# Optimization experiments

Hardware: AMD Instinct MI355X
Metric: run time of the kernel (lower is better)

The kernel has to match this reference:

```python
import jax, jax.numpy as jnp
import numpy as np

HID = 3584; NH = 16; NKV = 8; HD = 256; S = 3072; WIN = 2048
SOFTCAP = 50.0; QSCALE = 256.0 ** -0.5  # query_pre_attn_scalar = 256
NEG = -2.3819763e38


def _rope(x, cos, sin):
    # x: (B, S, heads, HD); cos/sin: (S, HD//2). Gemma half-split complex RoPE.
    x1, x2 = jnp.split(x, 2, axis=-1)
    c = cos[None, :, None, :]
    s = sin[None, :, None, :]
    return jnp.concatenate([x1 * c - x2 * s, x1 * s + x2 * c], axis=-1)


def setup_inputs() -> dict:
    key = jax.random.key(0)
    k1, k2, k3 = jax.random.split(key, 3)
    hidden_states = jax.random.normal(k1, (1, S, HID), jnp.float32)
    qkv_w = jax.random.normal(k2, (NH * HD + 2 * NKV * HD, HID), jnp.float32) * 0.02
    o_w = jax.random.normal(k3, (HID, NH * HD), jnp.float32) * 0.02
    inv = 1.0 / (10000.0 ** (jnp.arange(0, HD, 2, dtype=jnp.float32) / HD))
    ang = jnp.arange(S, dtype=jnp.float32)[:, None] * inv[None, :]
    freqs_cis = jnp.stack([jnp.cos(ang), jnp.sin(ang)], axis=-1)  # (S, HD//2, 2)
    kv_write_indices = jnp.arange(S, dtype=jnp.int32)
    k_cache = jnp.zeros((1, S, NKV, HD), jnp.float32)
    v_cache = jnp.zeros((1, S, NKV, HD), jnp.float32)
    i = jnp.arange(S)[:, None]
    j = jnp.arange(S)[None, :]
    mask = jnp.where(j <= i, 0.0, NEG).astype(jnp.float32)[None, None]  # causal (1,1,S,S)
    return dict(hidden_states=hidden_states, freqs_cis=freqs_cis,
                kv_write_indices=kv_write_indices, k_cache=k_cache, v_cache=v_cache,
                mask=mask, qkv_w=qkv_w, o_w=o_w)


def reference(hidden_states, freqs_cis, kv_write_indices, k_cache, v_cache, mask, qkv_w, o_w):
    B, L, _ = hidden_states.shape
    qkv = hidden_states @ qkv_w.T  # (B, L, 8192)
    xq, xk, xv = jnp.split(qkv, [NH * HD, NH * HD + NKV * HD], axis=-1)
    xq = xq.reshape(B, L, NH, HD)
    xk = xk.reshape(B, L, NKV, HD)
    xv = xv.reshape(B, L, NKV, HD)
    cos, sin = freqs_cis[..., 0], freqs_cis[..., 1]
    xq = _rope(xq, cos, sin)
    xk = _rope(xk, cos, sin)
    # KV cache index_copy_ on dim 1
    k_all = k_cache.at[:, kv_write_indices].set(xk)  # (B, T, NKV, HD)
    v_all = v_cache.at[:, kv_write_indices].set(xv)
    T = k_all.shape[1]
    G = NH // NKV  # queries per kv head; grouped einsum avoids repeat_interleave
    q = (xq * QSCALE).transpose(0, 2, 1, 3).reshape(B, NKV, G, L, HD)
    k = k_all.transpose(0, 2, 1, 3)  # (B, NKV, T, HD)
    v = v_all.transpose(0, 2, 1, 3)
    scores = jnp.einsum('bkgsd,bktd->bkgst', q, k)
    # logit softcapping
    scores = jnp.tanh(scores / SOFTCAP) * SOFTCAP
    # sliding-window band applied on top of the provided (causal) mask
    i = jnp.arange(L)[:, None]
    j = jnp.arange(T)[None, :]
    band = (j >= i - WIN + 1) & (j <= i + WIN - 1)
    m = jnp.where(band, mask, NEG)  # (1,1,L,T)
    scores = scores + m[:, :, None]  # broadcast over group dim
    probs = jax.nn.softmax(scores.astype(jnp.float32), axis=-1).astype(q.dtype)
    out = jnp.einsum('bkgst,bktd->bkgsd', probs, v)
    out = out.reshape(B, NH, L, HD).transpose(0, 2, 1, 3).reshape(B, L, NH * HD)
    return out @ o_w.T
```

## Files before the change

kernel.cpp:

```cpp
#include <hip/hip_runtime.h>

#define S_LEN 3072
#define NHQ 16
#define NKVH 8
#define HDIM 256
#define WIN 2048
#define QKV_COLS 8192

typedef __bf16 bf16x8 __attribute__((ext_vector_type(8)));
typedef float f32x4 __attribute__((ext_vector_type(4)));

__device__ __forceinline__ unsigned short f2bf(float f) {
    union { float f; unsigned u; } v; v.f = f;
    unsigned r = v.u + 0x7FFFu + ((v.u >> 16) & 1u);
    return (unsigned short)(r >> 16);
}
__device__ __forceinline__ float bf2f(unsigned short u) {
    union { unsigned u; float f; } v; v.u = ((unsigned)u) << 16; return v.f;
}

typedef __attribute__((address_space(3))) void lds_void_t;
typedef const __attribute__((address_space(1))) void glb_void_t;
__device__ __forceinline__ void async16(const void* g, void* l) {
    __builtin_amdgcn_global_load_lds((glb_void_t*)g, (lds_void_t*)l, 16, 0, 0);
}

__global__ __launch_bounds__(256) void cast_bf16_kernel(const float* __restrict__ src,
                                                        unsigned short* __restrict__ dst,
                                                        int n) {
    int i = (blockIdx.x * 256 + threadIdx.x) * 4;
    if (i >= n) return;
    float4 v = *(const float4*)(src + i);
    ushort4 o;
    o.x = f2bf(v.x); o.y = f2bf(v.y); o.z = f2bf(v.z); o.w = f2bf(v.w);
    *(ushort4*)(dst + i) = o;
}

template <int OUT_BF16>
__global__ __launch_bounds__(256) void gemm_bt(const unsigned short* __restrict__ A,
                                               const unsigned short* __restrict__ B,
                                               void* __restrict__ Cv,
                                               int N, int K) {
    __shared__ __align__(16) unsigned short At[128 * 32];
    __shared__ __align__(16) unsigned short Bt[128 * 32];
    const int tid = threadIdx.x;
    const int wid = tid >> 6, lane = tid & 63;
    const int ln = lane & 15, quad = lane >> 4;
    const int bm = blockIdx.y, bn = blockIdx.x;
    const int wm = wid >> 1, wn = wid & 1;

    const f32x4 fzero = {0.f, 0.f, 0.f, 0.f};
    f32x4 acc[4][4];
#pragma unroll
    for (int i = 0; i < 4; i++) {
#pragma unroll
        for (int j = 0; j < 4; j++) acc[i][j] = fzero;
    }

    const unsigned short* gA = A + (size_t)(bm * 128 + wid * 32 + (lane >> 2)) * K + (lane & 3) * 8;
    const unsigned short* gB = B + (size_t)(bn * 128 + wid * 32 + (lane >> 2)) * K + (lane & 3) * 8;
    unsigned short* lA = At + wid * 32 * 32;
    unsigned short* lB = Bt + wid * 32 * 32;

    for (int k0 = 0; k0 < K; k0 += 32) {
        async16(gA + k0, lA);
        async16(gA + k0 + 16 * K, lA + 16 * 32);
        async16(gB + k0, lB);
        async16(gB + k0 + 16 * K, lB + 16 * 32);
        __syncthreads();

        bf16x8 af[4], bfr[4];
#pragma unroll
        for (int mt = 0; mt < 4; mt++)
            af[mt] = *(const bf16x8*)(At + (wm * 64 + mt * 16 + ln) * 32 + quad * 8);
#pragma unroll
        for (int nt = 0; nt < 4; nt++)
            bfr[nt] = *(const bf16x8*)(Bt + (wn * 64 + nt * 16 + ln) * 32 + quad * 8);
#pragma unroll
        for (int mt = 0; mt < 4; mt++) {
#pragma unroll
            for (int nt = 0; nt < 4; nt++)
                acc[mt][nt] = __builtin_amdgcn_mfma_f32_16x16x32_bf16(af[mt], bfr[nt], acc[mt][nt], 0, 0, 0);
        }
        __syncthreads();
    }

    const int row0 = bm * 128 + wm * 64 + quad * 4;
    const int col0 = bn * 128 + wn * 64 + ln;
    if (OUT_BF16) {
        unsigned short* C = (unsigned short*)Cv;
#pragma unroll
        for (int mt = 0; mt < 4; mt++) {
#pragma unroll
            for (int nt = 0; nt < 4; nt++) {
#pragma unroll
                for (int rr = 0; rr < 4; rr++)
                    C[(size_t)(row0 + mt * 16 + rr) * N + col0 + nt * 16] = f2bf(acc[mt][nt][rr]);
            }
        }
    } else {
        float* C = (float*)Cv;
#pragma unroll
        for (int mt = 0; mt < 4; mt++) {
#pragma unroll
            for (int nt = 0; nt < 4; nt++) {
#pragma unroll
                for (int rr = 0; rr < 4; rr++)
                    C[(size_t)(row0 + mt * 16 + rr) * N + col0 + nt * 16] = acc[mt][nt][rr];
            }
        }
    }
}

__global__ __launch_bounds__(256) void rope_kernel(const unsigned short* __restrict__ qkv,
                                                   const float* __restrict__ freqs,
                                                   const int* __restrict__ kvidx,
                                                   unsigned short* __restrict__ Qb,
                                                   unsigned short* __restrict__ Kb) {
    int t = blockIdx.x * 256 + threadIdx.x;
    int d = t & 127;
    int t2 = t >> 7;
    int hh = t2 % 24;
    int pos = t2 / 24;
    if (pos >= S_LEN) return;
    float2 cs = *(const float2*)(freqs + ((size_t)pos * 128 + d) * 2);
    if (hh < NHQ) {
        const unsigned short* src = qkv + (size_t)pos * QKV_COLS + hh * HDIM + d;
        float x1 = bf2f(src[0]), x2 = bf2f(src[128]);
        float o1 = (x1 * cs.x - x2 * cs.y) * 0.0625f;
        float o2 = (x1 * cs.y + x2 * cs.x) * 0.0625f;
        unsigned short* dst = Qb + ((size_t)hh * S_LEN + pos) * HDIM + d;
        dst[0] = f2bf(o1);
        dst[128] = f2bf(o2);
    } else {
        int kvh = hh - NHQ;
        const unsigned short* src = qkv + (size_t)pos * QKV_COLS + NHQ * HDIM + kvh * HDIM + d;
        float x1 = bf2f(src[0]), x2 = bf2f(src[128]);
        float o1 = x1 * cs.x - x2 * cs.y;
        float o2 = x1 * cs.y + x2 * cs.x;
        int wpos = kvidx[pos];
        unsigned short* dst = Kb + ((size_t)kvh * S_LEN + wpos) * HDIM + d;
        dst[0] = f2bf(o1);
        dst[128] = f2bf(o2);
    }
}

__global__ __launch_bounds__(256) void vtrans_kernel(const unsigned short* __restrict__ qkv,
                                                     const int* __restrict__ kvidx,
                                                     unsigned short* __restrict__ Vbt) {
    __shared__ unsigned short T[64][72];
    int pos0 = blockIdx.x * 64;
    int c0 = blockIdx.y * 64;
    int a = threadIdx.x >> 6;
    int b = threadIdx.x & 63;
#pragma unroll
    for (int r = 0; r < 16; r++) {
        int pl = r * 4 + a;
        T[pl][b] = qkv[(size_t)(pos0 + pl) * QKV_COLS + 6144 + c0 + b];
    }
    __syncthreads();
    int wpos = kvidx[pos0 + b];
#pragma unroll
    for (int r = 0; r < 16; r++) {
        int cl = r * 4 + a;
        Vbt[(size_t)(c0 + cl) * S_LEN + wpos] = T[b][cl];
    }
}

__global__ __launch_bounds__(256) void attn_kernel(const unsigned short* __restrict__ Qb,
                                                   const unsigned short* __restrict__ Kb,
                                                   const unsigned short* __restrict__ Vbt,
                                                   float* __restrict__ Acc,
                                                   float* __restrict__ Ps,
                                                   unsigned short* __restrict__ attn_out) {
    __shared__ __align__(16) unsigned short Kl[32][264];
    __shared__ __align__(16) unsigned short Vt[256][40];
    __shared__ __align__(16) unsigned short Pl[4][16][40];

    const int h = blockIdx.x / 96;
    const int it = 95 - (blockIdx.x % 96);
    int qb, sub, nc;
    if (it < 16)      { qb = it; sub = 0; nc = 1; }
    else if (it < 48) { int e = it - 16; qb = 16 + (e >> 1); sub = e & 1; nc = 2; }
    else              { int e = it - 48; qb = 32 + e / 3; sub = e % 3; nc = 3; }

    const int kv = h >> 1;
    const int q0 = qb * 64;
    const int tid = threadIdx.x;
    const int wid = tid >> 6, lane = tid & 63;
    const int ln = lane & 15, quad = lane >> 4;

    bf16x8 qf[8];
    {
        const unsigned short* qrow = Qb + ((size_t)h * S_LEN + q0 + wid * 16 + ln) * HDIM;
#pragma unroll
        for (int k0 = 0; k0 < 8; k0++)
            qf[k0] = *(const bf16x8*)(qrow + k0 * 32 + quad * 8);
    }

    const f32x4 fzero = {0.f, 0.f, 0.f, 0.f};
    f32x4 acc[16];
#pragma unroll
    for (int t = 0; t < 16; t++) acc[t] = fzero;
    float ps[4] = {0.f, 0.f, 0.f, 0.f};

    const int imin = q0 + wid * 16;
    const int imax = imin + 15;
    const int irow = imin + quad * 4;

    const int t_lo = (q0 >= WIN) ? ((q0 - (WIN - 1)) >> 5) : 0;
    const int t_hi = (q0 + 63) >> 5;
    const int tn = t_hi - t_lo + 1;
    const int ts = t_lo + (tn * sub) / nc;
    const int te = t_lo + (tn * (sub + 1)) / nc;

    const int krow = tid >> 3, kcs = (tid & 7) * 32;
    const unsigned short* ksrc0 = Kb + ((size_t)kv * S_LEN + krow) * HDIM + kcs;
    const unsigned short* vsrc0 = Vbt + ((size_t)kv * HDIM + tid) * S_LEN;

    for (int tt = ts; tt < te; tt++) {
        const int p0 = tt * 32;
        {
            const unsigned short* ks = ksrc0 + (size_t)p0 * HDIM;
            unsigned short* kd = &Kl[krow][kcs];
#pragma unroll
            for (int j = 0; j < 4; j++)
                *(uint4*)(kd + j * 8) = *(const uint4*)(ks + j * 8);
            const unsigned short* vs = vsrc0 + p0;
            unsigned short* vd = &Vt[tid][0];
#pragma unroll
            for (int j = 0; j < 4; j++)
                *(uint4*)(vd + j * 8) = *(const uint4*)(vs + j * 8);
        }
        __syncthreads();

        const bool live = (p0 <= imax) && (p0 + 31 >= imin - WIN + 1);
        if (live) {
            f32x4 s0 = fzero, s1 = fzero;
#pragma unroll
            for (int k0 = 0; k0 < 8; k0++) {
                bf16x8 b0 = *(const bf16x8*)(&Kl[ln][k0 * 32 + quad * 8]);
                s0 = __builtin_amdgcn_mfma_f32_16x16x32_bf16(qf[k0], b0, s0, 0, 0, 0);
            }
#pragma unroll
            for (int k0 = 0; k0 < 8; k0++) {
                bf16x8 b1 = *(const bf16x8*)(&Kl[16 + ln][k0 * 32 + quad * 8]);
                s1 = __builtin_amdgcn_mfma_f32_16x16x32_bf16(qf[k0], b1, s1, 0, 0, 0);
            }

            const bool full = (p0 + 31 <= imin) && (p0 >= imax - WIN + 1);
#pragma unroll
            for (int r = 0; r < 4; r++) {
                float z0 = __expf(s0[r] * 0.04f);
                float z1 = __expf(s1[r] * 0.04f);
                float t0 = fmaf(-100.f, __builtin_amdgcn_rcpf(z0 + 1.f), 50.f);
                float t1 = fmaf(-100.f, __builtin_amdgcn_rcpf(z1 + 1.f), 50.f);
                float p0v = __expf(t0);
                float p1v = __expf(t1);
                if (!full) {
                    const int i = irow + r;
                    int j0 = p0 + ln, j1 = p0 + 16 + ln;
                    p0v = ((j0 <= i) && (j0 + WIN > i)) ? p0v : 0.f;
                    p1v = ((j1 <= i) && (j1 + WIN > i)) ? p1v : 0.f;
                }
                ps[r] += p0v + p1v;
                Pl[wid][quad * 4 + r][ln] = f2bf(p0v);
                Pl[wid][quad * 4 + r][16 + ln] = f2bf(p1v);
            }
            bf16x8 pa = *(const bf16x8*)(&Pl[wid][ln][quad * 8]);
#pragma unroll
            for (int t = 0; t < 16; t++) {
                bf16x8 vb = *(const bf16x8*)(&Vt[t * 16 + ln][quad * 8]);
                acc[t] = __builtin_amdgcn_mfma_f32_16x16x32_bf16(pa, vb, acc[t], 0, 0, 0);
            }
        }
        __syncthreads();
    }

    float psr[4];
#pragma unroll
    for (int r = 0; r < 4; r++) {
        float s = ps[r];
#pragma unroll
        for (int o = 1; o <= 8; o <<= 1)
            s += __shfl_xor(s, o);
        psr[r] = s;
    }

    if (nc == 1) {
#pragma unroll
        for (int t = 0; t < 16; t++) {
#pragma unroll
            for (int r = 0; r < 4; r++) {
                float o = acc[t][r] * __builtin_amdgcn_rcpf(psr[r]);
                attn_out[(size_t)(irow + r) * 4096 + h * HDIM + t * 16 + ln] = f2bf(o);
            }
        }
    } else {
        if (ln == 0) {
#pragma unroll
            for (int r = 0; r < 4; r++)
                atomicAdd(&Ps[h * S_LEN + irow + r], psr[r]);
        }
#pragma unroll
        for (int t = 0; t < 16; t++) {
#pragma unroll
            for (int r = 0; r < 4; r++)
                atomicAdd(&Acc[((size_t)h * S_LEN + irow + r) * HDIM + t * 16 + ln], acc[t][r]);
        }
    }
}

__global__ __launch_bounds__(256) void norm_kernel(const float* __restrict__ Acc,
                                                   const float* __restrict__ Ps,
                                                   unsigned short* __restrict__ attn_out) {
    int row = blockIdx.x * 4 + (threadIdx.x >> 6);
    int lane = threadIdx.x & 63;
    int h = row >> 11;
    int pos = 1024 + (row & 2047);
    float4 a = *(const float4*)(Acc + ((size_t)h * S_LEN + pos) * HDIM + lane * 4);
    float inv = __builtin_amdgcn_rcpf(Ps[h * S_LEN + pos]);
    ushort4 o;
    o.x = f2bf(a.x * inv); o.y = f2bf(a.y * inv);
    o.z = f2bf(a.z * inv); o.w = f2bf(a.w * inv);
    *(ushort4*)(attn_out + (size_t)pos * 4096 + h * HDIM + lane * 4) = o;
}

extern "C" void kernel_launch(void* const* d_in, const int* in_sizes, int n_in,
                              void* d_out, int out_size, void* d_ws, size_t ws_size,
                              hipStream_t stream) {
    (void)in_sizes; (void)n_in; (void)out_size; (void)ws_size;
    const float* hidden = (const float*)d_in[0];
    const float* freqs  = (const float*)d_in[1];
    const int* kvidx    = (const int*)d_in[2];
    const float* qkv_w  = (const float*)d_in[6];
    const float* o_w    = (const float*)d_in[7];
    float* out = (float*)d_out;

    char* ws = (char*)d_ws;
    unsigned short* hs_bf   = (unsigned short*)(ws);
    unsigned short* w1_bf   = (unsigned short*)(ws + 22020096);
    unsigned short* w2_bf   = (unsigned short*)(ws + 80740352);
    unsigned short* qkv_bf  = (unsigned short*)(ws + 110100480);
    unsigned short* Qb      = (unsigned short*)(ws + 160432128);
    unsigned short* Kb      = (unsigned short*)(ws + 185597952);
    unsigned short* Vbt     = (unsigned short*)(ws + 198180864);
    unsigned short* attn_bf = (unsigned short*)(ws + 210763776);

    float* Acc = (float*)(ws + 110100480);
    float* Ps  = (float*)(ws);

    cast_bf16_kernel<<<10752, 256, 0, stream>>>(hidden, hs_bf, 11010048);
    cast_bf16_kernel<<<28672, 256, 0, stream>>>(qkv_w, w1_bf, 29360128);
    cast_bf16_kernel<<<14336, 256, 0, stream>>>(o_w, w2_bf, 14680064);

    gemm_bt<1><<<dim3(64, 24), 256, 0, stream>>>(hs_bf, w1_bf, (void*)qkv_bf, 8192, 3584);

    rope_kernel<<<36864, 256, 0, stream>>>(qkv_bf, freqs, kvidx, Qb, Kb);
    vtrans_kernel<<<dim3(48, 32), 256, 0, stream>>>(qkv_bf, kvidx, Vbt);

    hipMemsetAsync(Acc, 0, (size_t)16 * 3072 * 256 * 4, stream);
    hipMemsetAsync(Ps, 0, (size_t)16 * 3072 * 4, stream);

    attn_kernel<<<1536, 256, 0, stream>>>(Qb, Kb, Vbt, Acc, Ps, attn_bf);
    norm_kernel<<<8192, 256, 0, stream>>>(Acc, Ps, attn_bf);

    gemm_bt<0><<<dim3(28, 24), 256, 0, stream>>>(attn_bf, w2_bf, (void*)out, 3584, 4096);
}
```

Baseline: 942.7 us.

## Make attention waves independent with 32-row tiles reading K/V directly from global

Restructures the attention kernel so each wave owns a 32-query-row tile and loads K and V fragments straight from global memory instead of staging them through shared memory. This removes the block-wide __syncthreads barriers. The work split now uses up to 5 KV chunks per tile, and the norm kernel covers the extra rows that need reduction. In exchange, each wave holds more registers (two Q fragment sets and two accumulator sets), relies on L2/cache for K/V reuse across waves, and does more atomic adds.

```diff
diff --git a/kernel.cpp b/kernel.cpp
--- a/kernel.cpp
+++ b/kernel.cpp
@@ -167,124 +167,121 @@
     }
 }
 
-__global__ __launch_bounds__(256) void attn_kernel(const unsigned short* __restrict__ Qb,
-                                                   const unsigned short* __restrict__ Kb,
-                                                   const unsigned short* __restrict__ Vbt,
-                                                   float* __restrict__ Acc,
-                                                   float* __restrict__ Ps,
-                                                   unsigned short* __restrict__ attn_out) {
-    __shared__ __align__(16) unsigned short Kl[32][264];
-    __shared__ __align__(16) unsigned short Vt[256][40];
-    __shared__ __align__(16) unsigned short Pl[4][16][40];
-
-    const int h = blockIdx.x / 96;
-    const int it = 95 - (blockIdx.x % 96);
-    int qb, sub, nc;
-    if (it < 16)      { qb = it; sub = 0; nc = 1; }
-    else if (it < 48) { int e = it - 16; qb = 16 + (e >> 1); sub = e & 1; nc = 2; }
-    else              { int e = it - 48; qb = 32 + e / 3; sub = e % 3; nc = 3; }
-
-    const int kv = h >> 1;
-    const int q0 = qb * 64;
+__global__ __launch_bounds__(256, 2) void attn_kernel(const unsigned short* __restrict__ Qb,
+                                                      const unsigned short* __restrict__ Kb,
+                                                      const unsigned short* __restrict__ Vbt,
+                                                      float* __restrict__ Acc,
+                                                      float* __restrict__ Ps,
+                                                      unsigned short* __restrict__ attn_out) {
+    __shared__ __align__(16) unsigned short Pl[4][2][16][40];
+
     const int tid = threadIdx.x;
     const int wid = tid >> 6, lane = tid & 63;
     const int ln = lane & 15, quad = lane >> 4;
 
-    bf16x8 qf[8];
-    {
-        const unsigned short* qrow = Qb + ((size_t)h * S_LEN + q0 + wid * 16 + ln) * HDIM;
-#pragma unroll
-        for (int k0 = 0; k0 < 8; k0++)
-            qf[k0] = *(const bf16x8*)(qrow + k0 * 32 + quad * 8);
-    }
-
-    const f32x4 fzero = {0.f, 0.f, 0.f, 0.f};
-    f32x4 acc[16];
-#pragma unroll
-    for (int t = 0; t < 16; t++) acc[t] = fzero;
-    float ps[4] = {0.f, 0.f, 0.f, 0.f};
-
-    const int imin = q0 + wid * 16;
-    const int imax = imin + 15;
-    const int irow = imin + quad * 4;
-
-    const int t_lo = (q0 >= WIN) ? ((q0 - (WIN - 1)) >> 5) : 0;
-    const int t_hi = (q0 + 63) >> 5;
-    const int tn = t_hi - t_lo + 1;
+    const int w = 5119 - (blockIdx.x * 4 + wid);
+    const int h = w / 320;
+    const int rem = w % 320;
+    int qt, sub, nc;
+    if (rem < 16)       { qt = rem; sub = 0; nc = 1; }
+    else if (rem < 48)  { int e = rem - 16;  qt = 16 + (e >> 1); sub = e & 1; nc = 2; }
+    else if (rem < 96)  { int e = rem - 48;  qt = 32 + e / 3;    sub = e % 3; nc = 3; }
+    else if (rem < 160) { int e = rem - 96;  qt = 48 + (e >> 2); sub = e & 3; nc = 4; }
+    else                { int e = rem - 160; qt = 64 + e / 5;    sub = e % 5; nc = 5; }
+
+    const int kv = h >> 1;
+    const int imin = qt * 32;
+    const int imax = imin + 31;
+
+    const int t_lo = (qt > 64) ? (qt - 64) : 0;
+    const int tn = qt - t_lo + 1;
     const int ts = t_lo + (tn * sub) / nc;
     const int te = t_lo + (tn * (sub + 1)) / nc;
 
-    const int krow = tid >> 3, kcs = (tid & 7) * 32;
-    const unsigned short* ksrc0 = Kb + ((size_t)kv * S_LEN + krow) * HDIM + kcs;
-    const unsigned short* vsrc0 = Vbt + ((size_t)kv * HDIM + tid) * S_LEN;
+    bf16x8 qf0[8], qf1[8];
+    {
+        const unsigned short* q0p = Qb + ((size_t)h * S_LEN + imin + ln) * HDIM + quad * 8;
+#pragma unroll
+        for (int k0 = 0; k0 < 8; k0++) qf0[k0] = *(const bf16x8*)(q0p + k0 * 32);
+        const unsigned short* q1p = q0p + 16 * HDIM;
+#pragma unroll
+        for (int k0 = 0; k0 < 8; k0++) qf1[k0] = *(const bf16x8*)(q1p + k0 * 32);
+    }
+
+    const f32x4 fzero = {0.f, 0.f, 0.f, 0.f};
+    f32x4 acc0[16], acc1[16];
+#pragma unroll
+    for (int t = 0; t < 16; t++) { acc0[t] = fzero; acc1[t] = fzero; }
+    float ps0[4] = {0.f, 0.f, 0.f, 0.f};
+    float ps1[4] = {0.f, 0.f, 0.f, 0.f};
+
+    const unsigned short* kbase = Kb + ((size_t)kv * S_LEN + ln) * HDIM + quad * 8;
+    const unsigned short* vbase = Vbt + ((size_t)kv * HDIM + ln) * S_LEN + quad * 8;
 
     for (int tt = ts; tt < te; tt++) {
         const int p0 = tt * 32;
+
+        f32x4 s00 = fzero, s10 = fzero, s01 = fzero, s11 = fzero;
         {
-            const unsigned short* ks = ksrc0 + (size_t)p0 * HDIM;
-            unsigned short* kd = &Kl[krow][kcs];
-#pragma unroll
-            for (int j = 0; j < 4; j++)
-                *(uint4*)(kd + j * 8) = *(const uint4*)(ks + j * 8);
-            const unsigned short* vs = vsrc0 + p0;
-            unsigned short* vd = &Vt[tid][0];
-#pragma unroll
-            for (int j = 0; j < 4; j++)
-                *(uint4*)(vd + j * 8) = *(const uint4*)(vs + j * 8);
-        }
-        __syncthreads();
-
-        const bool live = (p0 <= imax) && (p0 + 31 >= imin - WIN + 1);
-        if (live) {
-            f32x4 s0 = fzero, s1 = fzero;
+            const unsigned short* kp = kbase + (size_t)p0 * HDIM;
 #pragma unroll
             for (int k0 = 0; k0 < 8; k0++) {
-                bf16x8 b0 = *(const bf16x8*)(&Kl[ln][k0 * 32 + quad * 8]);
-                s0 = __builtin_amdgcn_mfma_f32_16x16x32_bf16(qf[k0], b0, s0, 0, 0, 0);
-            }
+                bf16x8 kf = *(const bf16x8*)(kp + k0 * 32);
+                s00 = __builtin_amdgcn_mfma_f32_16x16x32_bf16(qf0[k0], kf, s00, 0, 0, 0);
+                s10 = __builtin_amdgcn_mfma_f32_16x16x32_bf16(qf1[k0], kf, s10, 0, 0, 0);
+            }
+            const unsigned short* kp1 = kp + 16 * HDIM;
 #pragma unroll
             for (int k0 = 0; k0 < 8; k0++) {
-                bf16x8 b1 = *(const bf16x8*)(&Kl[16 + ln][k0 * 32 + quad * 8]);
-                s1 = __builtin_amdgcn_mfma_f32_16x16x32_bf16(qf[k0], b1, s1, 0, 0, 0);
-            }
-
-            const bool full = (p0 + 31 <= imin) && (p0 >= imax - WIN + 1);
+                bf16x8 kf = *(const bf16x8*)(kp1 + k0 * 32);
+                s01 = __builtin_amdgcn_mfma_f32_16x16x32_bf16(qf0[k0], kf, s01, 0, 0, 0);
+                s11 = __builtin_amdgcn_mfma_f32_16x16x32_bf16(qf1[k0], kf, s11, 0, 0, 0);
+            }
+        }
+
+        const bool full = (p0 + 31 <= imin) && (p0 >= imax - WIN + 1);
+#pragma unroll
+        for (int m = 0; m < 2; m++) {
+            f32x4 sa = m ? s10 : s00;
+            f32x4 sb = m ? s11 : s01;
+            float* ps = m ? ps1 : ps0;
 #pragma unroll
             for (int r = 0; r < 4; r++) {
-                float z0 = __expf(s0[r] * 0.04f);
-                float z1 = __expf(s1[r] * 0.04f);
+                float z0 = __expf(sa[r] * 0.04f);
+                float z1 = __expf(sb[r] * 0.04f);
                 float t0 = fmaf(-100.f, __builtin_amdgcn_rcpf(z0 + 1.f), 50.f);
                 float t1 = fmaf(-100.f, __builtin_amdgcn_rcpf(z1 + 1.f), 50.f);
                 float p0v = __expf(t0);
                 float p1v = __expf(t1);
                 if (!full) {
-                    const int i = irow + r;
+                    const int i = imin + m * 16 + quad * 4 + r;
                     int j0 = p0 + ln, j1 = p0 + 16 + ln;
                     p0v = ((j0 <= i) && (j0 + WIN > i)) ? p0v : 0.f;
                     p1v = ((j1 <= i) && (j1 + WIN > i)) ? p1v : 0.f;
                 }
                 ps[r] += p0v + p1v;
-                Pl[wid][quad * 4 + r][ln] = f2bf(p0v);
-                Pl[wid][quad * 4 + r][16 + ln] = f2bf(p1v);
-            }
-            bf16x8 pa = *(const bf16x8*)(&Pl[wid][ln][quad * 8]);
-#pragma unroll
-            for (int t = 0; t < 16; t++) {
-                bf16x8 vb = *(const bf16x8*)(&Vt[t * 16 + ln][quad * 8]);
-                acc[t] = __builtin_amdgcn_mfma_f32_16x16x32_bf16(pa, vb, acc[t], 0, 0, 0);
-            }
-        }
-        __syncthreads();
-    }
-
-    float psr[4];
+                Pl[wid][m][quad * 4 + r][ln] = f2bf(p0v);
+                Pl[wid][m][quad * 4 + r][16 + ln] = f2bf(p1v);
+            }
+        }
+        bf16x8 pa0 = *(const bf16x8*)(&Pl[wid][0][ln][quad * 8]);
+        bf16x8 pa1 = *(const bf16x8*)(&Pl[wid][1][ln][quad * 8]);
+        const unsigned short* vp = vbase + p0;
+#pragma unroll
+        for (int t = 0; t < 16; t++) {
+            bf16x8 vb = *(const bf16x8*)(vp + (size_t)t * 16 * S_LEN);
+            acc0[t] = __builtin_amdgcn_mfma_f32_16x16x32_bf16(pa0, vb, acc0[t], 0, 0, 0);
+            acc1[t] = __builtin_amdgcn_mfma_f32_16x16x32_bf16(pa1, vb, acc1[t], 0, 0, 0);
+        }
+    }
+
+    float psr0[4], psr1[4];
 #pragma unroll
     for (int r = 0; r < 4; r++) {
-        float s = ps[r];
-#pragma unroll
-        for (int o = 1; o <= 8; o <<= 1)
-            s += __shfl_xor(s, o);
-        psr[r] = s;
+        float a = ps0[r], b = ps1[r];
+#pragma unroll
+        for (int o = 1; o <= 8; o <<= 1) { a += __shfl_xor(a, o); b += __shfl_xor(b, o); }
+        psr0[r] = a; psr1[r] = b;
     }
 
     if (nc == 1) {
@@ -292,21 +289,29 @@
         for (int t = 0; t < 16; t++) {
 #pragma unroll
             for (int r = 0; r < 4; r++) {
-                float o = acc[t][r] * __builtin_amdgcn_rcpf(psr[r]);
-                attn_out[(size_t)(irow + r) * 4096 + h * HDIM + t * 16 + ln] = f2bf(o);
+                int i0 = imin + quad * 4 + r;
+                attn_out[(size_t)i0 * 4096 + h * HDIM + t * 16 + ln] =
+                    f2bf(acc0[t][r] * __builtin_amdgcn_rcpf(psr0[r]));
+                attn_out[(size_t)(i0 + 16) * 4096 + h * HDIM + t * 16 + ln] =
+                    f2bf(acc1[t][r] * __builtin_amdgcn_rcpf(psr1[r]));
             }
         }
     } else {
         if (ln == 0) {
 #pragma unroll
-            for (int r = 0; r < 4; r++)
-                atomicAdd(&Ps[h * S_LEN + irow + r], psr[r]);
+            for (int r = 0; r < 4; r++) {
+                atomicAdd(&Ps[h * S_LEN + imin + quad * 4 + r], psr0[r]);
+                atomicAdd(&Ps[h * S_LEN + imin + 16 + quad * 4 + r], psr1[r]);
+            }
         }
 #pragma unroll
         for (int t = 0; t < 16; t++) {
 #pragma unroll
-            for (int r = 0; r < 4; r++)
-                atomicAdd(&Acc[((size_t)h * S_LEN + irow + r) * HDIM + t * 16 + ln], acc[t][r]);
+            for (int r = 0; r < 4; r++) {
+                int i0 = imin + quad * 4 + r;
+                atomicAdd(&Acc[((size_t)h * S_LEN + i0) * HDIM + t * 16 + ln], acc0[t][r]);
+                atomicAdd(&Acc[((size_t)h * S_LEN + i0 + 16) * HDIM + t * 16 + ln], acc1[t][r]);
+            }
         }
     }
 }
@@ -316,8 +321,8 @@
                                                    unsigned short* __restrict__ attn_out) {
     int row = blockIdx.x * 4 + (threadIdx.x >> 6);
     int lane = threadIdx.x & 63;
-    int h = row >> 11;
-    int pos = 1024 + (row & 2047);
+    int h = row / 2560;
+    int pos = 512 + (row % 2560);
     float4 a = *(const float4*)(Acc + ((size_t)h * S_LEN + pos) * HDIM + lane * 4);
     float inv = __builtin_amdgcn_rcpf(Ps[h * S_LEN + pos]);
     ushort4 o;
@@ -362,8 +367,8 @@
     hipMemsetAsync(Acc, 0, (size_t)16 * 3072 * 256 * 4, stream);
     hipMemsetAsync(Ps, 0, (size_t)16 * 3072 * 4, stream);
 
-    attn_kernel<<<1536, 256, 0, stream>>>(Qb, Kb, Vbt, Acc, Ps, attn_bf);
-    norm_kernel<<<8192, 256, 0, stream>>>(Acc, Ps, attn_bf);
+    attn_kernel<<<1280, 256, 0, stream>>>(Qb, Kb, Vbt, Acc, Ps, attn_bf);
+    norm_kernel<<<10240, 256, 0, stream>>>(Acc, Ps, attn_bf);
 
     gemm_bt<0><<<dim3(28, 24), 256, 0, stream>>>(attn_bf, w2_bf, (void*)out, 3584, 4096);
 }
```

New measurement: 1.146 ms. 21.6% more time.
